# Kernel optimization log

Hardware: AMD Instinct MI355X
Metric: run time of the kernel (lower is better)

Reference implementation:

```python
import jax, jax.numpy as jnp
import numpy as np

GROUP = 64  # quantization group size along the input dim


def dequantize(W_q, scale, zero):
    """int4 dequant: W_q uint8-packed [out, in/2] (two nibbles per byte),
    group-wise affine scale/zero [out, in/GROUP]. Returns float [out, in]."""
    out, half = W_q.shape
    hi = (W_q >> 4) & 0xF
    lo = W_q & 0xF
    w = jnp.stack([hi, lo], axis=-1).reshape(out, half * 2).astype(scale.dtype)
    w = w.reshape(out, -1, GROUP)  # [out, n_groups, GROUP]
    w = (w - zero[:, :, None]) * scale[:, :, None]
    return w.reshape(out, half * 2)


def setup_inputs() -> dict:
    key = jax.random.key(0)
    ks = jax.random.split(key, 10)
    hidden, inter = 4096, 11008
    B, S = 4, 1024
    x = jax.random.normal(ks[0], (B, S, hidden), dtype=jnp.float32)
    gate_Wq = jax.random.randint(ks[1], (inter, hidden // 2), 0, 256, dtype=jnp.int32)
    up_Wq = jax.random.randint(ks[2], (inter, hidden // 2), 0, 256, dtype=jnp.int32)
    down_Wq = jax.random.randint(ks[3], (hidden, inter // 2), 0, 256, dtype=jnp.int32)
    # small scales keep activations sane; zero points in [0, 15]
    gate_scale = jax.random.uniform(ks[4], (inter, hidden // GROUP)) * 0.01 + 1e-4
    gate_zero = jax.random.uniform(ks[5], (inter, hidden // GROUP)) * 15.0
    up_scale = jax.random.uniform(ks[6], (inter, hidden // GROUP)) * 0.01 + 1e-4
    up_zero = jax.random.uniform(ks[7], (inter, hidden // GROUP)) * 15.0
    down_scale = jax.random.uniform(ks[8], (hidden, inter // GROUP)) * 0.01 + 1e-4
    down_zero = jax.random.uniform(ks[9], (hidden, inter // GROUP)) * 15.0
    return {"x": x, "gate_Wq": gate_Wq, "up_Wq": up_Wq, "down_Wq": down_Wq,
            "gate_scale": gate_scale, "gate_zero": gate_zero,
            "up_scale": up_scale, "up_zero": up_zero,
            "down_scale": down_scale, "down_zero": down_zero}


def reference(x, gate_Wq, up_Wq, down_Wq, gate_scale, gate_zero,
              up_scale, up_zero, down_scale, down_zero):
    Wg = dequantize(gate_Wq, gate_scale, gate_zero)  # [inter, hidden]
    Wu = dequantize(up_Wq, up_scale, up_zero)        # [inter, hidden]
    Wd = dequantize(down_Wq, down_scale, down_zero)  # [hidden, inter]
    g = jnp.einsum('bsh,ih->bsi', x, Wg)
    u = jnp.einsum('bsh,ih->bsi', x, Wu)
    h = jax.nn.silu(g) * u
    return jnp.einsum('bsi,hi->bsh', h, Wd)
```

## Files before the change

kernel.cpp:

```cpp
#include <hip/hip_runtime.h>
#include <hip/hip_fp16.h>
#include <cstdint>
#include <cstddef>

#define HIDDEN 4096
#define INTER  11008
#define NTOK   4096
#define NG1    (HIDDEN/64)
#define NG2    (INTER/64)

typedef _Float16 f16;
typedef _Float16 f16x8 __attribute__((ext_vector_type(8)));
typedef float    f32x4 __attribute__((ext_vector_type(4)));

__device__ __forceinline__ void g2lds16(const void* g, void* l) {
  __builtin_amdgcn_global_load_lds(
      (const __attribute__((address_space(1))) uint32_t*)g,
      (__attribute__((address_space(3))) uint32_t*)l, 16, 0, 0);
}

__device__ __forceinline__ uint32_t dq2(uint32_t b, __half2 s2, __half2 nzs) {
  uint32_t qb = 0x64006400u | (b >> 4) | ((b & 0xFu) << 16);
  __half2 hq = __builtin_bit_cast(__half2, qb);
  __half2 t  = __hsub2(hq, __builtin_bit_cast(__half2, 0x64006400u));
  __half2 wv = __hfma2(t, s2, nzs);
  return __builtin_bit_cast(uint32_t, wv);
}

__global__ __launch_bounds__(256) void cvt_x(const float* __restrict__ x,
                                             f16* __restrict__ xh) {
  size_t i = ((size_t)blockIdx.x * 256 + threadIdx.x) * 8;
  float4 a = *(const float4*)(x + i);
  float4 b = *(const float4*)(x + i + 4);
  f16x8 o = {(f16)a.x, (f16)a.y, (f16)a.z, (f16)a.w,
             (f16)b.x, (f16)b.y, (f16)b.z, (f16)b.w};
  *(f16x8*)(xh + i) = o;
}

__global__ __launch_bounds__(256) void deq_w(const uint32_t* __restrict__ q,
                                             const float* __restrict__ s,
                                             const float* __restrict__ z,
                                             f16* __restrict__ out) {
  int g = blockIdx.x * 256 + threadIdx.x;
  const uint32_t* qp = q + (size_t)g * 32;
  float sf = s[g], zf = z[g];
  __half2 s2 = __float2half2_rn(sf), nzs = __float2half2_rn(-zf * sf);
  f16* op = out + (size_t)g * 64;
#pragma unroll
  for (int i = 0; i < 8; ++i) {
    uint4 w = *(const uint4*)(qp + i * 4);
    uint4 o;
    o.x = dq2(w.x, s2, nzs); o.y = dq2(w.y, s2, nzs);
    o.z = dq2(w.z, s2, nzs); o.w = dq2(w.w, s2, nzs);
    *(uint4*)(op + i * 8) = o;
  }
}


__global__ __launch_bounds__(512, 2) void gemm_gateup2(
    const f16* __restrict__ xh, const f16* __restrict__ wg,
    const f16* __restrict__ wu, f16* __restrict__ h) {
  extern __shared__ char smem[];
  const int tid = threadIdx.x, lane = tid & 63, wave = tid >> 6;
  const int bm = blockIdx.x, bn = blockIdx.y;
  const int wm = wave >> 2, wn = wave & 3;

  const int srow = tid >> 3;
  const int sk8  = (tid & 7) ^ (srow & 7);
  const f16* aptr = xh + (size_t)(bm * 256 + srow) * HIDDEN + sk8 * 8;
  const f16* gptr = wg + (size_t)(bn * 128 + srow) * HIDDEN + sk8 * 8;
  const f16* uptr = wu + (size_t)(bn * 128 + srow) * HIDDEN + sk8 * 8;
  const int soff = tid * 16;

  int abase[8], asel[8];
#pragma unroll
  for (int im = 0; im < 8; ++im) {
    int r = wm * 128 + im * 16 + (lane & 15);
    abase[im] = r * 128; asel[im] = r & 7;
  }
  int bbase[4], bsel[4];
#pragma unroll
  for (int in_ = 0; in_ < 4; ++in_) {
    int r = wn * 64 + in_ * 16 + (lane & 15);
    bbase[in_] = 32768 + r * 128; bsel[in_] = r & 7;
  }
  const int kchunk = lane >> 4;

  f32x4 acc[8][4] = {};

  auto stage = [&](int kt, int pb) {
    char* base = smem + pb * 65536;
    const f16* ap = aptr + (size_t)kt * 64;
#pragma unroll
    for (int i = 0; i < 4; ++i)
      g2lds16(ap + (size_t)i * 64 * HIDDEN, base + soff + i * 8192);
    const f16* gp = gptr + (size_t)kt * 64;
    g2lds16(gp,                           base + 32768 + soff);
    g2lds16(gp + (size_t)64 * HIDDEN,     base + 32768 + soff + 8192);
    const f16* up = uptr + (size_t)kt * 64;
    g2lds16(up,                           base + 32768 + soff + 16384);
    g2lds16(up + (size_t)64 * HIDDEN,     base + 32768 + soff + 24576);
  };
  auto compute = [&](int pb) {
    const char* base = smem + pb * 65536;
#pragma unroll
    for (int ks = 0; ks < 2; ++ks) {
      int kc = ks * 4 + kchunk;
      f16x8 a[8], b[4];
#pragma unroll
      for (int im = 0; im < 8; ++im)
        a[im] = *(const f16x8*)(base + abase[im] + ((kc ^ asel[im]) << 4));
#pragma unroll
      for (int in_ = 0; in_ < 4; ++in_)
        b[in_] = *(const f16x8*)(base + bbase[in_] + ((kc ^ bsel[in_]) << 4));
#pragma unroll
      for (int im = 0; im < 8; ++im)
#pragma unroll
        for (int in_ = 0; in_ < 4; ++in_)
          acc[im][in_] = __builtin_amdgcn_mfma_f32_16x16x32_f16(a[im], b[in_], acc[im][in_], 0, 0, 0);
    }
  };

  stage(0, 0);
  __syncthreads();

  for (int kt = 0; kt < NG1 - 1; ++kt) {
    stage(kt + 1, (kt + 1) & 1);
    __builtin_amdgcn_sched_barrier(0);
    compute(kt & 1);
    __syncthreads();
  }
  compute((NG1 - 1) & 1);

  const int r0 = (lane >> 4) * 4;
  const int c0 = lane & 15;
  if (wn < 2) {
    char* reg = smem + (wm * 2 + wn) * 16384;
#pragma unroll
    for (int im = 0; im < 8; ++im)
#pragma unroll
      for (int in_ = 0; in_ < 4; ++in_)
#pragma unroll
        for (int r = 0; r < 4; ++r) {
          float g = acc[im][in_][r];
          float sg = g / (1.0f + __expf(-g));
          int rowL = im * 16 + r0 + r, colL = in_ * 16 + c0;
          *(f16*)(reg + rowL * 128 + colL * 2) = (f16)sg;
        }
  }
  __syncthreads();
  if (wn >= 2) {
    const char* reg = smem + (wm * 2 + (wn - 2)) * 16384;
#pragma unroll
    for (int im = 0; im < 8; ++im)
#pragma unroll
      for (int in_ = 0; in_ < 4; ++in_)
#pragma unroll
        for (int r = 0; r < 4; ++r) {
          int rowL = im * 16 + r0 + r, colL = in_ * 16 + c0;
          float sg = (float)*(const f16*)(reg + rowL * 128 + colL * 2);
          float hv = sg * acc[im][in_][r];
          int row = bm * 256 + wm * 128 + rowL;
          int col = bn * 128 + (wn - 2) * 64 + colL;
          h[(size_t)row * INTER + col] = (f16)hv;
        }
  }
}

__global__ __launch_bounds__(512, 2) void gemm_down2(
    const f16* __restrict__ h, const f16* __restrict__ wd,
    float* __restrict__ out) {
  extern __shared__ char smem[];
  const int tid = threadIdx.x, lane = tid & 63, wave = tid >> 6;
  const int bm = blockIdx.x, bn = blockIdx.y;
  const int wm = wave >> 2, wn = wave & 3;

  const int srow = tid >> 3;
  const int sk8  = (tid & 7) ^ (srow & 7);
  const f16* aptr = h  + (size_t)(bm * 256 + srow) * INTER + sk8 * 8;
  const f16* bptr = wd + (size_t)(bn * 256 + srow) * INTER + sk8 * 8;
  const int soff = tid * 16;

  int abase[8], asel[8];
#pragma unroll
  for (int im = 0; im < 8; ++im) {
    int r = wm * 128 + im * 16 + (lane & 15);
    abase[im] = r * 128; asel[im] = r & 7;
  }
  int bbase[4], bsel[4];
#pragma unroll
  for (int in_ = 0; in_ < 4; ++in_) {
    int r = wn * 64 + in_ * 16 + (lane & 15);
    bbase[in_] = 32768 + r * 128; bsel[in_] = r & 7;
  }
  const int kchunk = lane >> 4;

  f32x4 acc[8][4] = {};

  auto stage = [&](int kt, int pb) {
    char* base = smem + pb * 65536;
    const f16* ap = aptr + (size_t)kt * 64;
    const f16* bp = bptr + (size_t)kt * 64;
#pragma unroll
    for (int i = 0; i < 4; ++i) {
      g2lds16(ap + (size_t)i * 64 * INTER, base + soff + i * 8192);
      g2lds16(bp + (size_t)i * 64 * INTER, base + 32768 + soff + i * 8192);
    }
  };
  auto compute = [&](int pb) {
    const char* base = smem + pb * 65536;
#pragma unroll
    for (int ks = 0; ks < 2; ++ks) {
      int kc = ks * 4 + kchunk;
      f16x8 a[8], b[4];
#pragma unroll
      for (int im = 0; im < 8; ++im)
        a[im] = *(const f16x8*)(base + abase[im] + ((kc ^ asel[im]) << 4));
#pragma unroll
      for (int in_ = 0; in_ < 4; ++in_)
        b[in_] = *(const f16x8*)(base + bbase[in_] + ((kc ^ bsel[in_]) << 4));
#pragma unroll
      for (int im = 0; im < 8; ++im)
#pragma unroll
        for (int in_ = 0; in_ < 4; ++in_)
          acc[im][in_] = __builtin_amdgcn_mfma_f32_16x16x32_f16(a[im], b[in_], acc[im][in_], 0, 0, 0);
    }
  };

  stage(0, 0);
  __syncthreads();
  for (int kt = 0; kt < NG2 - 1; ++kt) {
    stage(kt + 1, (kt + 1) & 1);
    __builtin_amdgcn_sched_barrier(0);
    compute(kt & 1);
    __syncthreads();
  }
  compute((NG2 - 1) & 1);

  const int r0 = (lane >> 4) * 4;
  const int c0 = lane & 15;
#pragma unroll
  for (int im = 0; im < 8; ++im)
#pragma unroll
    for (int in_ = 0; in_ < 4; ++in_)
#pragma unroll
      for (int r = 0; r < 4; ++r) {
        int row = bm * 256 + wm * 128 + im * 16 + r0 + r;
        int col = bn * 256 + wn * 64 + in_ * 16 + c0;
        out[(size_t)row * HIDDEN + col] = acc[im][in_][r];
      }
}

__global__ __launch_bounds__(512, 4) void gemm_gateup_q(
    const f16* __restrict__ xh,
    const uint32_t* __restrict__ gq, const uint32_t* __restrict__ uq,
    const float* __restrict__ gs, const float* __restrict__ gz,
    const float* __restrict__ us, const float* __restrict__ uz,
    f16* __restrict__ h) {
  extern __shared__ char smem[];
  f16* lA0 = (f16*)smem;
  f16* lA1 = (f16*)(smem + 32768);
  char* lBg = smem + 65536;
  char* lBu = smem + 73728;
  const int tid = threadIdx.x, lane = tid & 63, wave = tid >> 6;
  const int bm = blockIdx.x, bn = blockIdx.y;
  const int wm = wave >> 1, wn = wave & 1;

  const int arow0 = tid >> 3;
  const int ak8s  = (tid & 7) ^ (arow0 & 7);
  const f16* aptr = xh + (size_t)(bm * 256 + arow0) * HIDDEN + ak8s * 8;
  const int aoff = tid * 16;

  const int mat = tid >> 8;
  const int t = tid & 255;
  const int brow0 = t >> 3;
  const uint32_t* qp = (mat ? uq : gq) + (size_t)(bn * 64 + brow0) * (HIDDEN / 2) + (t & 7) * 4;
  const float* sp = (mat ? us : gs) + (size_t)(bn * 64 + brow0) * NG1;
  const float* zp = (mat ? uz : gz) + (size_t)(bn * 64 + brow0) * NG1;
  char* lb = mat ? lBu : lBg;
  const int bws0 = brow0 * 128 + (((t & 7) ^ (brow0 & 7)) << 4);

  int abase[4], asel[4];
#pragma unroll
  for (int im = 0; im < 4; ++im) {
    int r = wm * 64 + im * 16 + (lane & 15);
    abase[im] = r * 128; asel[im] = r & 7;
  }
  int bbase[2], bsel[2];
#pragma unroll
  for (int in_ = 0; in_ < 2; ++in_) {
    int r = wn * 32 + in_ * 16 + (lane & 15);
    bbase[in_] = r * 128; bsel[in_] = r & 7;
  }
  const int kchunk = lane >> 4;

  f32x4 accg[4][2] = {};
  f32x4 accu[4][2] = {};

  auto stageA = [&](const f16* src, f16* dst) {
#pragma unroll
    for (int i = 0; i < 4; ++i)
      g2lds16(src + (size_t)i * 64 * HIDDEN, (char*)dst + aoff + i * 8192);
  };
  auto loadB = [&](int ktn, uint4& w0, uint4& w1,
                   float& s0f, float& z0f, float& s1f, float& z1f) {
    w0 = *(const uint4*)(qp + (size_t)ktn * 32);
    w1 = *(const uint4*)(qp + (size_t)32 * (HIDDEN / 2) + (size_t)ktn * 32);
    s0f = sp[ktn]; z0f = zp[ktn];
    s1f = sp[32 * NG1 + ktn]; z1f = zp[32 * NG1 + ktn];
  };
  auto writeB = [&](uint4 w0, uint4 w1, float s0f, float z0f, float s1f, float z1f) {
    __half2 s0 = __float2half2_rn(s0f), n0 = __float2half2_rn(-z0f * s0f);
    __half2 s1 = __float2half2_rn(s1f), n1 = __float2half2_rn(-z1f * s1f);
    uint4 o0, o1;
    o0.x = dq2(w0.x, s0, n0); o0.y = dq2(w0.y, s0, n0);
    o0.z = dq2(w0.z, s0, n0); o0.w = dq2(w0.w, s0, n0);
    o1.x = dq2(w1.x, s1, n1); o1.y = dq2(w1.y, s1, n1);
    o1.z = dq2(w1.z, s1, n1); o1.w = dq2(w1.w, s1, n1);
    *(uint4*)(lb + bws0) = o0;
    *(uint4*)(lb + bws0 + 32 * 128) = o1;
  };
  auto compute = [&](const f16* lA) {
#pragma unroll
    for (int ks = 0; ks < 2; ++ks) {
      int kc = ks * 4 + kchunk;
      f16x8 a[4], bg[2], bu[2];
#pragma unroll
      for (int im = 0; im < 4; ++im)
        a[im] = *(const f16x8*)((const char*)lA + abase[im] + ((kc ^ asel[im]) << 4));
#pragma unroll
      for (int in_ = 0; in_ < 2; ++in_) {
        bg[in_] = *(const f16x8*)(lBg + bbase[in_] + ((kc ^ bsel[in_]) << 4));
        bu[in_] = *(const f16x8*)(lBu + bbase[in_] + ((kc ^ bsel[in_]) << 4));
      }
#pragma unroll
      for (int im = 0; im < 4; ++im)
#pragma unroll
        for (int in_ = 0; in_ < 2; ++in_) {
          accg[im][in_] = __builtin_amdgcn_mfma_f32_16x16x32_f16(a[im], bg[in_], accg[im][in_], 0, 0, 0);
          accu[im][in_] = __builtin_amdgcn_mfma_f32_16x16x32_f16(a[im], bu[in_], accu[im][in_], 0, 0, 0);
        }
    }
  };

  stageA(aptr, lA0);
  {
    uint4 w0, w1; float s0f, z0f, s1f, z1f;
    loadB(0, w0, w1, s0f, z0f, s1f, z1f);
    writeB(w0, w1, s0f, z0f, s1f, z1f);
  }
  __syncthreads();

  for (int kt = 0; kt < NG1 - 1; ++kt) {
    stageA(aptr + (size_t)(kt + 1) * 64, (kt & 1) ? lA0 : lA1);
    uint4 w0, w1; float s0f, z0f, s1f, z1f;
    loadB(kt + 1, w0, w1, s0f, z0f, s1f, z1f);
    compute((kt & 1) ? lA1 : lA0);
    __syncthreads();
    writeB(w0, w1, s0f, z0f, s1f, z1f);
    __syncthreads();
  }
  compute(((NG1 - 1) & 1) ? lA1 : lA0);

#pragma unroll
  for (int im = 0; im < 4; ++im)
#pragma unroll
    for (int in_ = 0; in_ < 2; ++in_)
#pragma unroll
      for (int r = 0; r < 4; ++r) {
        int row = bm * 256 + wm * 64 + im * 16 + (lane >> 4) * 4 + r;
        int col = bn * 64 + wn * 32 + in_ * 16 + (lane & 15);
        float g = accg[im][in_][r];
        float u = accu[im][in_][r];
        float hv = (g / (1.0f + __expf(-g))) * u;
        h[(size_t)row * INTER + col] = (f16)hv;
      }
}

__global__ __launch_bounds__(512, 4) void gemm_down_q(
    const f16* __restrict__ h, const uint32_t* __restrict__ dq_,
    const float* __restrict__ dsc, const float* __restrict__ dz,
    float* __restrict__ out) {
  extern __shared__ char smem[];
  f16* lA0 = (f16*)smem;
  f16* lA1 = (f16*)(smem + 32768);
  char* lB = smem + 65536;
  const int tid = threadIdx.x, lane = tid & 63, wave = tid >> 6;
  const int bm = blockIdx.x, bn = blockIdx.y;
  const int wm = wave >> 1, wn = wave & 1;

  const int arow0 = tid >> 3;
  const int ak8s  = (tid & 7) ^ (arow0 & 7);
  const f16* aptr = h + (size_t)(bm * 256 + arow0) * INTER + ak8s * 8;
  const int aoff = tid * 16;

  const int brow0 = tid >> 3;
  const uint32_t* qp = dq_ + (size_t)(bn * 128 + brow0) * (INTER / 2) + (tid & 7) * 4;
  const float* sp = dsc + (size_t)(bn * 128 + brow0) * NG2;
  const float* zp = dz + (size_t)(bn * 128 + brow0) * NG2;
  const int bws0 = brow0 * 128 + (((tid & 7) ^ (brow0 & 7)) << 4);

  int abase[4], asel[4];
#pragma unroll
  for (int im = 0; im < 4; ++im) {
    int r = wm * 64 + im * 16 + (lane & 15);
    abase[im] = r * 128; asel[im] = r & 7;
  }
  int bbase[4], bsel[4];
#pragma unroll
  for (int in_ = 0; in_ < 4; ++in_) {
    int r = wn * 64 + in_ * 16 + (lane & 15);
    bbase[in_] = r * 128; bsel[in_] = r & 7;
  }
  const int kchunk = lane >> 4;

  f32x4 acc[4][4] = {};

  auto stageA = [&](const f16* src, f16* dst) {
#pragma unroll
    for (int i = 0; i < 4; ++i)
      g2lds16(src + (size_t)i * 64 * INTER, (char*)dst + aoff + i * 8192);
  };
  auto loadB = [&](int ktn, uint4& w0, uint4& w1,
                   float& s0f, float& z0f, float& s1f, float& z1f) {
    w0 = *(const uint4*)(qp + (size_t)ktn * 32);
    w1 = *(const uint4*)(qp + (size_t)64 * (INTER / 2) + (size_t)ktn * 32);
    s0f = sp[ktn]; z0f = zp[ktn];
    s1f = sp[64 * NG2 + ktn]; z1f = zp[64 * NG2 + ktn];
  };
  auto writeB = [&](uint4 w0, uint4 w1, float s0f, float z0f, float s1f, float z1f) {
    __half2 s0 = __float2half2_rn(s0f), n0 = __float2half2_rn(-z0f * s0f);
    __half2 s1 = __float2half2_rn(s1f), n1 = __float2half2_rn(-z1f * s1f);
    uint4 o0, o1;
    o0.x = dq2(w0.x, s0, n0); o0.y = dq2(w0.y, s0, n0);
    o0.z = dq2(w0.z, s0, n0); o0.w = dq2(w0.w, s0, n0);
    o1.x = dq2(w1.x, s1, n1); o1.y = dq2(w1.y, s1, n1);
    o1.z = dq2(w1.z, s1, n1); o1.w = dq2(w1.w, s1, n1);
    *(uint4*)(lB + bws0) = o0;
    *(uint4*)(lB + bws0 + 64 * 128) = o1;
  };
  auto compute = [&](const f16* lA) {
#pragma unroll
    for (int ks = 0; ks < 2; ++ks) {
      int kc = ks * 4 + kchunk;
      f16x8 a[4], b[4];
#pragma unroll
      for (int im = 0; im < 4; ++im)
        a[im] = *(const f16x8*)((const char*)lA + abase[im] + ((kc ^ asel[im]) << 4));
#pragma unroll
      for (int in_ = 0; in_ < 4; ++in_)
        b[in_] = *(const f16x8*)(lB + bbase[in_] + ((kc ^ bsel[in_]) << 4));
#pragma unroll
      for (int im = 0; im < 4; ++im)
#pragma unroll
        for (int in_ = 0; in_ < 4; ++in_)
          acc[im][in_] = __builtin_amdgcn_mfma_f32_16x16x32_f16(a[im], b[in_], acc[im][in_], 0, 0, 0);
    }
  };

  stageA(aptr, lA0);
  {
    uint4 w0, w1; float s0f, z0f, s1f, z1f;
    loadB(0, w0, w1, s0f, z0f, s1f, z1f);
    writeB(w0, w1, s0f, z0f, s1f, z1f);
  }
  __syncthreads();

  for (int kt = 0; kt < NG2 - 1; ++kt) {
    stageA(aptr + (size_t)(kt + 1) * 64, (kt & 1) ? lA0 : lA1);
    uint4 w0, w1; float s0f, z0f, s1f, z1f;
    loadB(kt + 1, w0, w1, s0f, z0f, s1f, z1f);
    compute((kt & 1) ? lA1 : lA0);
    __syncthreads();
    writeB(w0, w1, s0f, z0f, s1f, z1f);
    __syncthreads();
  }
  compute(((NG2 - 1) & 1) ? lA1 : lA0);

#pragma unroll
  for (int im = 0; im < 4; ++im)
#pragma unroll
    for (int in_ = 0; in_ < 4; ++in_)
#pragma unroll
      for (int r = 0; r < 4; ++r) {
        int row = bm * 256 + wm * 64 + im * 16 + (lane >> 4) * 4 + r;
        int col = bn * 128 + wn * 64 + in_ * 16 + (lane & 15);
        out[(size_t)row * HIDDEN + col] = acc[im][in_][r];
      }
}

extern "C" void kernel_launch(void* const* d_in, const int* in_sizes, int n_in,
                              void* d_out, int out_size, void* d_ws, size_t ws_size,
                              hipStream_t stream) {
  const float*    x   = (const float*)d_in[0];
  const uint32_t* gq  = (const uint32_t*)d_in[1];
  const uint32_t* uq  = (const uint32_t*)d_in[2];
  const uint32_t* dqw = (const uint32_t*)d_in[3];
  const float*    gs  = (const float*)d_in[4];
  const float*    gz  = (const float*)d_in[5];
  const float*    us  = (const float*)d_in[6];
  const float*    uz  = (const float*)d_in[7];
  const float*    dsc = (const float*)d_in[8];
  const float*    dzz = (const float*)d_in[9];

  const size_t XH = (size_t)NTOK * HIDDEN * 2;
  const size_t HB = (size_t)NTOK * INTER * 2;
  const size_t WB = (size_t)INTER * HIDDEN * 2;
  f16* xh   = (f16*)d_ws;
  f16* hbuf = (f16*)((char*)d_ws + XH);
  float* out = (float*)d_out;

  cvt_x<<<dim3((NTOK * HIDDEN) / (256 * 8)), 256, 0, stream>>>(x, xh);

  if (ws_size >= XH + HB + 2 * WB) {
    f16* W1 = (f16*)((char*)d_ws + XH + HB);
    f16* W2 = (f16*)((char*)d_ws + XH + HB + WB);
    const int LDS_BIG = 128 * 1024;
    (void)hipFuncSetAttribute((const void*)gemm_gateup2,
                              hipFuncAttributeMaxDynamicSharedMemorySize, LDS_BIG);
    (void)hipFuncSetAttribute((const void*)gemm_down2,
                              hipFuncAttributeMaxDynamicSharedMemorySize, LDS_BIG);
    deq_w<<<dim3((INTER * NG1) / 256), 256, 0, stream>>>(gq, gs, gz, W1);
    deq_w<<<dim3((INTER * NG1) / 256), 256, 0, stream>>>(uq, us, uz, W2);
    gemm_gateup2<<<dim3(NTOK / 256, INTER / 128), 512, LDS_BIG, stream>>>(
        xh, W1, W2, hbuf);
    deq_w<<<dim3((HIDDEN * NG2) / 256), 256, 0, stream>>>(dqw, dsc, dzz, W1);
    gemm_down2<<<dim3(NTOK / 256, HIDDEN / 256), 512, LDS_BIG, stream>>>(
        hbuf, W1, out);
  } else {
    const int LDS_Q = 80 * 1024;
    (void)hipFuncSetAttribute((const void*)gemm_gateup_q,
                              hipFuncAttributeMaxDynamicSharedMemorySize, LDS_Q);
    (void)hipFuncSetAttribute((const void*)gemm_down_q,
                              hipFuncAttributeMaxDynamicSharedMemorySize, LDS_Q);
    gemm_gateup_q<<<dim3(NTOK / 256, INTER / 64), 512, LDS_Q, stream>>>(
        xh, gq, uq, gs, gz, us, uz, hbuf);
    gemm_down_q<<<dim3(NTOK / 256, HIDDEN / 128), 512, LDS_Q, stream>>>(
        hbuf, dqw, dsc, dzz, out);
  }
}
```

Before: 1.446 ms.

## Replace full syncthreads with partial vmcnt waits, add MFMA priority, swizzle epilogue LDS

In both fp16 GEMM kernels, the full __syncthreads at each k-step is replaced by split barriers. One waits only until the older stage's global-to-LDS loads land (vmcnt(8)), so the next tile's prefetch stays in flight during compute. The other waits only on LDS reads before the buffer is reused. MFMA blocks are wrapped in s_setprio to favour matrix issue across waves. The gate/up epilogue's silu staging in LDS gets an XOR swizzle to cut bank conflicts. The hand-written waitcnt counts depend on the exact number of outstanding loads per stage, so a wrong count would cause a race.

```diff
diff --git a/kernel.cpp b/kernel.cpp
--- a/kernel.cpp
+++ b/kernel.cpp
@@ -17,6 +17,22 @@
   __builtin_amdgcn_global_load_lds(
       (const __attribute__((address_space(1))) uint32_t*)g,
       (__attribute__((address_space(3))) uint32_t*)l, 16, 0, 0);
+}
+
+__device__ __forceinline__ void bar_vm8() {
+  asm volatile("s_waitcnt vmcnt(8)" ::: "memory");
+  __builtin_amdgcn_s_barrier();
+  asm volatile("" ::: "memory");
+}
+__device__ __forceinline__ void bar_lgkm() {
+  asm volatile("s_waitcnt lgkmcnt(0)" ::: "memory");
+  __builtin_amdgcn_s_barrier();
+  asm volatile("" ::: "memory");
+}
+__device__ __forceinline__ void bar_vm0() {
+  asm volatile("s_waitcnt vmcnt(0)" ::: "memory");
+  __builtin_amdgcn_s_barrier();
+  asm volatile("" ::: "memory");
 }
 
 __device__ __forceinline__ uint32_t dq2(uint32_t b, __half2 s2, __half2 nzs) {
@@ -113,26 +129,29 @@
 #pragma unroll
       for (int in_ = 0; in_ < 4; ++in_)
         b[in_] = *(const f16x8*)(base + bbase[in_] + ((kc ^ bsel[in_]) << 4));
+      __builtin_amdgcn_s_setprio(1);
 #pragma unroll
       for (int im = 0; im < 8; ++im)
 #pragma unroll
         for (int in_ = 0; in_ < 4; ++in_)
           acc[im][in_] = __builtin_amdgcn_mfma_f32_16x16x32_f16(a[im], b[in_], acc[im][in_], 0, 0, 0);
+      __builtin_amdgcn_s_setprio(0);
     }
   };
 
   stage(0, 0);
-  __syncthreads();
 
   for (int kt = 0; kt < NG1 - 1; ++kt) {
     stage(kt + 1, (kt + 1) & 1);
     __builtin_amdgcn_sched_barrier(0);
+    bar_vm8();
     compute(kt & 1);
-    __syncthreads();
-  }
+    bar_lgkm();
+  }
+  bar_vm0();
   compute((NG1 - 1) & 1);
 
-  const int r0 = (lane >> 4) * 4;
+  const int q4 = (lane >> 4) * 4;
   const int c0 = lane & 15;
   if (wn < 2) {
     char* reg = smem + (wm * 2 + wn) * 16384;
@@ -144,8 +163,9 @@
         for (int r = 0; r < 4; ++r) {
           float g = acc[im][in_][r];
           float sg = g / (1.0f + __expf(-g));
-          int rowL = im * 16 + r0 + r, colL = in_ * 16 + c0;
-          *(f16*)(reg + rowL * 128 + colL * 2) = (f16)sg;
+          int rowL = im * 16 + q4 + r;
+          int off = rowL * 128 + ((in_ ^ ((rowL >> 2) & 3)) << 5) + c0 * 2;
+          *(f16*)(reg + off) = (f16)sg;
         }
   }
   __syncthreads();
@@ -157,11 +177,12 @@
       for (int in_ = 0; in_ < 4; ++in_)
 #pragma unroll
         for (int r = 0; r < 4; ++r) {
-          int rowL = im * 16 + r0 + r, colL = in_ * 16 + c0;
-          float sg = (float)*(const f16*)(reg + rowL * 128 + colL * 2);
+          int rowL = im * 16 + q4 + r;
+          int off = rowL * 128 + ((in_ ^ ((rowL >> 2) & 3)) << 5) + c0 * 2;
+          float sg = (float)*(const f16*)(reg + off);
           float hv = sg * acc[im][in_][r];
           int row = bm * 256 + wm * 128 + rowL;
-          int col = bn * 128 + (wn - 2) * 64 + colL;
+          int col = bn * 128 + (wn - 2) * 64 + in_ * 16 + c0;
           h[(size_t)row * INTER + col] = (f16)hv;
         }
   }
@@ -219,22 +240,25 @@
 #pragma unroll
       for (int in_ = 0; in_ < 4; ++in_)
         b[in_] = *(const f16x8*)(base + bbase[in_] + ((kc ^ bsel[in_]) << 4));
+      __builtin_amdgcn_s_setprio(1);
 #pragma unroll
       for (int im = 0; im < 8; ++im)
 #pragma unroll
         for (int in_ = 0; in_ < 4; ++in_)
           acc[im][in_] = __builtin_amdgcn_mfma_f32_16x16x32_f16(a[im], b[in_], acc[im][in_], 0, 0, 0);
+      __builtin_amdgcn_s_setprio(0);
     }
   };
 
   stage(0, 0);
-  __syncthreads();
   for (int kt = 0; kt < NG2 - 1; ++kt) {
     stage(kt + 1, (kt + 1) & 1);
     __builtin_amdgcn_sched_barrier(0);
+    bar_vm8();
     compute(kt & 1);
-    __syncthreads();
-  }
+    bar_lgkm();
+  }
+  bar_vm0();
   compute((NG2 - 1) & 1);
 
   const int r0 = (lane >> 4) * 4;
```

Measured after the change: 1.497 ms. 1.04x slower.
